# Optimization experiments

Hardware: AMD Instinct MI355X
Metric: run time of the kernel (lower is better)

## Reference

```python
import jax, jax.numpy as jnp
import numpy as np

D_MODEL = 1024
NUM_HEADS = 16
DEPTH = D_MODEL // NUM_HEADS
B, S = 2, 2048


def setup_inputs() -> dict:
    key = jax.random.key(0)
    ks = jax.random.split(key, 11)
    sc = 1.0 / np.sqrt(D_MODEL)
    inp = {
        "q": jax.random.normal(ks[0], (B, S, D_MODEL), jnp.float32),
        "k": jax.random.normal(ks[1], (B, S, D_MODEL), jnp.float32),
        "v": jax.random.normal(ks[2], (B, S, D_MODEL), jnp.float32),
        # 1 = masked (upper triangle), broadcastable to [B,H,S,S]
        "mask": jnp.triu(jnp.ones((S, S), jnp.float32), k=1)[None, None],
        "wq": jax.random.normal(ks[3], (D_MODEL, D_MODEL), jnp.float32) * sc,
        "bq": jnp.zeros((D_MODEL,), jnp.float32),
        "wk": jax.random.normal(ks[4], (D_MODEL, D_MODEL), jnp.float32) * sc,
        "bk": jnp.zeros((D_MODEL,), jnp.float32),
        "wv": jax.random.normal(ks[5], (D_MODEL, D_MODEL), jnp.float32) * sc,
        "bv": jnp.zeros((D_MODEL,), jnp.float32),
        "wo": jax.random.normal(ks[6], (D_MODEL, D_MODEL), jnp.float32) * sc,
        "bo": jnp.zeros((D_MODEL,), jnp.float32),
    }
    return inp


def _split_heads(x):
    b, s, _ = x.shape
    return x.reshape(b, s, NUM_HEADS, DEPTH).transpose(0, 2, 1, 3)  # [B,H,S,D]


def reference(q, k, v, mask, wq, bq, wk, bk, wv, bv, wo, bo):
    qh = _split_heads(q @ wq + bq)
    kh = _split_heads(k @ wk + bk)
    vh = _split_heads(v @ wv + bv)
    logits = jnp.einsum("bhqd,bhkd->bhqk", qh, kh) / jnp.sqrt(
        jnp.asarray(DEPTH, qh.dtype))
    logits = logits + mask * (-1e9)
    attn = jax.nn.softmax(logits, axis=-1)  # [B,H,S,S]
    ctx = jnp.einsum("bhqk,bhkd->bhqd", attn, vh)
    concat = ctx.transpose(0, 2, 1, 3).reshape(q.shape[0], -1, D_MODEL)
    out = concat @ wo + bo
    return out, attn
```

## Files before the change

### kernel.cpp

```cpp
#include <hip/hip_runtime.h>
#include <cstdint>
#include <cstddef>

#define BATCH   2
#define SEQ     2048
#define DMODEL  1024
#define NHEADS  16
#define DHEAD   64
#define TOKENS  (BATCH*SEQ)

typedef __bf16 bf16_t;
typedef bf16_t bf16x8 __attribute__((ext_vector_type(8)));
typedef float  f32x4  __attribute__((ext_vector_type(4)));

__device__ __forceinline__ f32x4 mfma16(bf16x8 a, bf16x8 b, f32x4 c) {
    return __builtin_amdgcn_mfma_f32_16x16x32_bf16(a, b, c, 0, 0, 0);
}

template<int IN_BF16, int MODE>
__global__ __launch_bounds__(256, 2) void proj_gemm(
    const void* __restrict__ xin, const float* __restrict__ W,
    const float* __restrict__ bias, void* __restrict__ out)
{
    __shared__ __align__(16) bf16_t Xl[128*72];
    __shared__ __align__(16) bf16_t Wl[64*72];

    const int t    = threadIdx.x;
    const int w    = t >> 6;
    const int lane = t & 63;
    const int quad = lane >> 4;
    const int l16  = lane & 15;
    const int m0   = blockIdx.y * 128;
    const int n0   = blockIdx.x * 64;

    f32x4 acc[2][4] = {};

    for (int kt = 0; kt < DMODEL/64; ++kt) {
        __syncthreads();
        #pragma unroll
        for (int it = 0; it < 4; ++it) {
            int s   = t + it*256;
            int row = s >> 3, seg = s & 7;
            if (IN_BF16) {
                const bf16_t* xb = (const bf16_t*)xin + (size_t)(m0+row)*DMODEL + kt*64 + seg*8;
                *(bf16x8*)&Xl[row*72 + seg*8] = *(const bf16x8*)xb;
            } else {
                const float* xf = (const float*)xin + (size_t)(m0+row)*DMODEL + kt*64 + seg*8;
                float4 u0 = *(const float4*)xf;
                float4 u1 = *(const float4*)(xf + 4);
                bf16x8 vv;
                vv[0]=(bf16_t)u0.x; vv[1]=(bf16_t)u0.y; vv[2]=(bf16_t)u0.z; vv[3]=(bf16_t)u0.w;
                vv[4]=(bf16_t)u1.x; vv[5]=(bf16_t)u1.y; vv[6]=(bf16_t)u1.z; vv[7]=(bf16_t)u1.w;
                *(bf16x8*)&Xl[row*72 + seg*8] = vv;
            }
        }
        #pragma unroll
        for (int it = 0; it < 2; ++it) {
            int s    = t + it*256;
            int k    = s & 63;
            int nseg = s >> 6;
            const float* wp = W + (size_t)(kt*64 + k)*DMODEL + n0 + nseg*8;
            float4 u0 = *(const float4*)wp;
            float4 u1 = *(const float4*)(wp + 4);
            float f[8] = {u0.x,u0.y,u0.z,u0.w,u1.x,u1.y,u1.z,u1.w};
            #pragma unroll
            for (int j = 0; j < 8; ++j)
                Wl[(nseg*8 + j)*72 + k] = (bf16_t)f[j];
        }
        __syncthreads();

        #pragma unroll
        for (int kk = 0; kk < 2; ++kk) {
            bf16x8 a0 = *(const bf16x8*)&Xl[(w*32      + l16)*72 + kk*32 + quad*8];
            bf16x8 a1 = *(const bf16x8*)&Xl[(w*32 + 16 + l16)*72 + kk*32 + quad*8];
            #pragma unroll
            for (int c = 0; c < 4; ++c) {
                bf16x8 b = *(const bf16x8*)&Wl[(c*16 + l16)*72 + kk*32 + quad*8];
                acc[0][c] = mfma16(a0, b, acc[0][c]);
                acc[1][c] = mfma16(a1, b, acc[1][c]);
            }
        }
    }

    #pragma unroll
    for (int r = 0; r < 2; ++r) {
        #pragma unroll
        for (int c = 0; c < 4; ++c) {
            int n = n0 + c*16 + l16;
            float bv = bias[n];
            #pragma unroll
            for (int reg = 0; reg < 4; ++reg) {
                int gm = m0 + w*32 + r*16 + quad*4 + reg;
                float val = acc[r][c][reg] + bv;
                if (MODE == 2) {
                    ((float*)out)[(size_t)gm*DMODEL + n] = val;
                } else {
                    int b = gm >> 11, sTok = gm & (SEQ-1);
                    int h = n >> 6,  d    = n & (DHEAD-1);
                    if (MODE == 0)
                        ((bf16_t*)out)[(((size_t)(b*NHEADS + h))*SEQ + sTok)*DHEAD + d] = (bf16_t)val;
                    else
                        ((bf16_t*)out)[(((size_t)(b*NHEADS + h))*DHEAD + d)*SEQ + sTok] = (bf16_t)val;
                }
            }
        }
    }
}

__global__ __launch_bounds__(256, 2) void attn_kernel(
    const bf16_t* __restrict__ Qh, const bf16_t* __restrict__ Kh,
    const bf16_t* __restrict__ Vt, float* __restrict__ attn,
    bf16_t* __restrict__ ctx)
{
    __shared__ __align__(16) bf16_t Ql[64*72];
    __shared__ __align__(16) bf16_t Kl[64*72];
    __shared__ __align__(16) bf16_t Vl[64*72];
    __shared__ __align__(16) bf16_t Pl[4][16*72];

    const int t    = threadIdx.x;
    const int w    = t >> 6;
    const int lane = t & 63;
    const int quad = lane >> 4;
    const int l16  = lane & 15;
    const int bh   = blockIdx.y;
    const int q0   = blockIdx.x * 64;

    const bf16_t* Qp = Qh + (size_t)bh * SEQ * DHEAD;
    const bf16_t* Kp = Kh + (size_t)bh * SEQ * DHEAD;
    const bf16_t* Vp = Vt + (size_t)bh * DHEAD * SEQ;
    float* attp = attn + (size_t)bh * SEQ * SEQ;

    #pragma unroll
    for (int it = 0; it < 2; ++it) {
        int s = t + it*256;
        int row = s >> 3, seg = s & 7;
        *(bf16x8*)&Ql[row*72 + seg*8] =
            *(const bf16x8*)(Qp + (size_t)(q0 + row)*DHEAD + seg*8);
    }
    __syncthreads();
    bf16x8 aq[2];
    aq[0] = *(const bf16x8*)&Ql[(w*16 + l16)*72 +      quad*8];
    aq[1] = *(const bf16x8*)&Ql[(w*16 + l16)*72 + 32 + quad*8];

    const int nkt = q0/64 + 1;
    const int qrow_base = q0 + w*16 + quad*4;

    float mrow[4] = {-1e30f, -1e30f, -1e30f, -1e30f};
    float lrow[4] = {0.f, 0.f, 0.f, 0.f};

    for (int kt = 0; kt < nkt; ++kt) {
        __syncthreads();
        #pragma unroll
        for (int it = 0; it < 2; ++it) {
            int s = t + it*256;
            int row = s >> 3, seg = s & 7;
            *(bf16x8*)&Kl[row*72 + seg*8] =
                *(const bf16x8*)(Kp + (size_t)(kt*64 + row)*DHEAD + seg*8);
        }
        __syncthreads();

        f32x4 sf[4] = {};
        #pragma unroll
        for (int kk = 0; kk < 2; ++kk) {
            #pragma unroll
            for (int c = 0; c < 4; ++c) {
                bf16x8 b = *(const bf16x8*)&Kl[(c*16 + l16)*72 + kk*32 + quad*8];
                sf[c] = mfma16(aq[kk], b, sf[c]);
            }
        }
        #pragma unroll
        for (int c = 0; c < 4; ++c) {
            int col = kt*64 + c*16 + l16;
            #pragma unroll
            for (int reg = 0; reg < 4; ++reg) {
                float sv = sf[c][reg] * 0.125f;
                if (col > qrow_base + reg) sv = -1e30f;
                sf[c][reg] = sv;
            }
        }
        #pragma unroll
        for (int reg = 0; reg < 4; ++reg) {
            float tm = fmaxf(fmaxf(sf[0][reg], sf[1][reg]), fmaxf(sf[2][reg], sf[3][reg]));
            #pragma unroll
            for (int msk = 1; msk < 16; msk <<= 1) tm = fmaxf(tm, __shfl_xor(tm, msk));
            float mnew = fmaxf(mrow[reg], tm);
            float ps = __expf(sf[0][reg] - mnew) + __expf(sf[1][reg] - mnew)
                     + __expf(sf[2][reg] - mnew) + __expf(sf[3][reg] - mnew);
            #pragma unroll
            for (int msk = 1; msk < 16; msk <<= 1) ps += __shfl_xor(ps, msk);
            lrow[reg] = lrow[reg] * __expf(mrow[reg] - mnew) + ps;
            mrow[reg] = mnew;
        }
    }

    float invl[4];
    #pragma unroll
    for (int reg = 0; reg < 4; ++reg) invl[reg] = 1.0f / lrow[reg];

    f32x4 cacc[4] = {};
    bf16_t* Plw = &Pl[w][0];

    for (int kt = 0; kt < nkt; ++kt) {
        __syncthreads();
        #pragma unroll
        for (int it = 0; it < 2; ++it) {
            int s = t + it*256;
            int row = s >> 3, seg = s & 7;
            *(bf16x8*)&Kl[row*72 + seg*8] =
                *(const bf16x8*)(Kp + (size_t)(kt*64 + row)*DHEAD + seg*8);
            *(bf16x8*)&Vl[row*72 + seg*8] =
                *(const bf16x8*)(Vp + (size_t)row*SEQ + kt*64 + seg*8);
        }
        __syncthreads();

        f32x4 sf[4] = {};
        #pragma unroll
        for (int kk = 0; kk < 2; ++kk) {
            #pragma unroll
            for (int c = 0; c < 4; ++c) {
                bf16x8 b = *(const bf16x8*)&Kl[(c*16 + l16)*72 + kk*32 + quad*8];
                sf[c] = mfma16(aq[kk], b, sf[c]);
            }
        }
        #pragma unroll
        for (int c = 0; c < 4; ++c) {
            int col = kt*64 + c*16 + l16;
            #pragma unroll
            for (int reg = 0; reg < 4; ++reg) {
                float sv = sf[c][reg] * 0.125f;
                float p  = (col > qrow_base + reg)
                             ? 0.0f
                             : __expf(sv - mrow[reg]) * invl[reg];
                attp[(size_t)(qrow_base + reg)*SEQ + col] = p;
                Plw[(quad*4 + reg)*72 + c*16 + l16] = (bf16_t)p;
            }
        }
        #pragma unroll
        for (int kk = 0; kk < 2; ++kk) {
            bf16x8 ap = *(const bf16x8*)&Plw[l16*72 + kk*32 + quad*8];
            #pragma unroll
            for (int c = 0; c < 4; ++c) {
                bf16x8 bv = *(const bf16x8*)&Vl[(c*16 + l16)*72 + kk*32 + quad*8];
                cacc[c] = mfma16(ap, bv, cacc[c]);
            }
        }
    }

    {
        int r = t >> 2;
        int c4base = nkt*16 + (t & 3);
        float4 z = make_float4(0.f, 0.f, 0.f, 0.f);
        float* rowp = attp + (size_t)(q0 + r)*SEQ;
        for (int c4 = c4base; c4 < SEQ/4; c4 += 4)
            ((float4*)rowp)[c4] = z;
    }

    const int b = bh >> 4, h = bh & 15;
    #pragma unroll
    for (int c = 0; c < 4; ++c) {
        #pragma unroll
        for (int reg = 0; reg < 4; ++reg) {
            int gq = qrow_base + reg;
            size_t idx = ((size_t)(b*SEQ + gq))*DMODEL + h*DHEAD + c*16 + l16;
            ctx[idx] = (bf16_t)cacc[c][reg];
        }
    }
}

extern "C" void kernel_launch(void* const* d_in, const int* in_sizes, int n_in,
                              void* d_out, int out_size, void* d_ws, size_t ws_size,
                              hipStream_t stream) {
    const float* q  = (const float*)d_in[0];
    const float* k  = (const float*)d_in[1];
    const float* v  = (const float*)d_in[2];
    const float* wq = (const float*)d_in[4];
    const float* bq = (const float*)d_in[5];
    const float* wk = (const float*)d_in[6];
    const float* bk = (const float*)d_in[7];
    const float* wv = (const float*)d_in[8];
    const float* bv = (const float*)d_in[9];
    const float* wo = (const float*)d_in[10];
    const float* bo = (const float*)d_in[11];

    float* out  = (float*)d_out;
    float* attn = out + (size_t)TOKENS * DMODEL;

    bf16_t* Qws = (bf16_t*)d_ws;
    bf16_t* Kws = Qws + (size_t)TOKENS * DMODEL;
    bf16_t* Vws = Kws + (size_t)TOKENS * DMODEL;
    bf16_t* Cws = Vws + (size_t)TOKENS * DMODEL;

    dim3 blk(256);
    dim3 gproj(DMODEL/64, TOKENS/128);
    proj_gemm<0,0><<<gproj, blk, 0, stream>>>(q, wq, bq, Qws);
    proj_gemm<0,0><<<gproj, blk, 0, stream>>>(k, wk, bk, Kws);
    proj_gemm<0,1><<<gproj, blk, 0, stream>>>(v, wv, bv, Vws);

    dim3 gattn(SEQ/64, BATCH*NHEADS);
    attn_kernel<<<gattn, blk, 0, stream>>>(Qws, Kws, Vws, attn, Cws);

    proj_gemm<1,2><<<gproj, blk, 0, stream>>>(Cws, wo, bo, out);
}
```

Baseline: 938.7 us.

## Pre-transpose weights to bf16, transpose QK tile layout, use exp2 and nontemporal stores

Adds a conv_w kernel that converts each fp32 weight matrix to a transposed bf16 copy, so the projection GEMMs can load W tiles with vectorized bf16x8 loads instead of a scalar-scatter fp32 conversion. The attention kernel swaps the MFMA operands so each lane owns a single query row. This cuts the row max/sum reductions to two shuffles, lets softmax use exp2f with a prescaled constant, and lets attention probabilities be written as float4 nontemporal stores. Scratch space for the converted weights reuses the attn output buffer and the Q workspace, which adds four small extra kernel launches and relies on ordering so that data is not overwritten while still in use.

Result: no change. 937.9 us (-0.1%).

```diff
diff --git a/kernel.cpp b/kernel.cpp
--- a/kernel.cpp
+++ b/kernel.cpp
@@ -11,15 +11,46 @@
 
 typedef __bf16 bf16_t;
 typedef bf16_t bf16x8 __attribute__((ext_vector_type(8)));
+typedef bf16_t bf16x4 __attribute__((ext_vector_type(4)));
 typedef float  f32x4  __attribute__((ext_vector_type(4)));
 
 __device__ __forceinline__ f32x4 mfma16(bf16x8 a, bf16x8 b, f32x4 c) {
     return __builtin_amdgcn_mfma_f32_16x16x32_bf16(a, b, c, 0, 0, 0);
 }
 
+__global__ __launch_bounds__(256) void conv_w(
+    const float* __restrict__ W, bf16_t* __restrict__ Wt)
+{
+    __shared__ bf16_t tl[64][65];
+    const int t  = threadIdx.x;
+    const int kb = blockIdx.y * 64;
+    const int nb = blockIdx.x * 64;
+    const int r  = t >> 2;
+    const int cs = (t & 3) * 16;
+
+    const float* src = W + (size_t)(kb + r)*DMODEL + nb + cs;
+    #pragma unroll
+    for (int j = 0; j < 4; ++j) {
+        float4 u = ((const float4*)src)[j];
+        tl[r][cs + j*4 + 0] = (bf16_t)u.x;
+        tl[r][cs + j*4 + 1] = (bf16_t)u.y;
+        tl[r][cs + j*4 + 2] = (bf16_t)u.z;
+        tl[r][cs + j*4 + 3] = (bf16_t)u.w;
+    }
+    __syncthreads();
+    bf16_t* dst = Wt + (size_t)(nb + r)*DMODEL + kb + cs;
+    #pragma unroll
+    for (int h = 0; h < 2; ++h) {
+        bf16x8 o;
+        #pragma unroll
+        for (int j = 0; j < 8; ++j) o[j] = tl[cs + h*8 + j][r];
+        *(bf16x8*)(dst + h*8) = o;
+    }
+}
+
 template<int IN_BF16, int MODE>
 __global__ __launch_bounds__(256, 2) void proj_gemm(
-    const void* __restrict__ xin, const float* __restrict__ W,
+    const void* __restrict__ xin, const bf16_t* __restrict__ Wt,
     const float* __restrict__ bias, void* __restrict__ out)
 {
     __shared__ __align__(16) bf16_t Xl[128*72];
@@ -56,16 +87,10 @@
         }
         #pragma unroll
         for (int it = 0; it < 2; ++it) {
-            int s    = t + it*256;
-            int k    = s & 63;
-            int nseg = s >> 6;
-            const float* wp = W + (size_t)(kt*64 + k)*DMODEL + n0 + nseg*8;
-            float4 u0 = *(const float4*)wp;
-            float4 u1 = *(const float4*)(wp + 4);
-            float f[8] = {u0.x,u0.y,u0.z,u0.w,u1.x,u1.y,u1.z,u1.w};
-            #pragma unroll
-            for (int j = 0; j < 8; ++j)
-                Wl[(nseg*8 + j)*72 + k] = (bf16_t)f[j];
+            int s = t + it*256;
+            int n = s >> 3, seg = s & 7;
+            *(bf16x8*)&Wl[n*72 + seg*8] =
+                *(const bf16x8*)(Wt + (size_t)(n0+n)*DMODEL + kt*64 + seg*8);
         }
         __syncthreads();
 
@@ -138,15 +163,15 @@
             *(const bf16x8*)(Qp + (size_t)(q0 + row)*DHEAD + seg*8);
     }
     __syncthreads();
-    bf16x8 aq[2];
-    aq[0] = *(const bf16x8*)&Ql[(w*16 + l16)*72 +      quad*8];
-    aq[1] = *(const bf16x8*)&Ql[(w*16 + l16)*72 + 32 + quad*8];
-
-    const int nkt = q0/64 + 1;
-    const int qrow_base = q0 + w*16 + quad*4;
-
-    float mrow[4] = {-1e30f, -1e30f, -1e30f, -1e30f};
-    float lrow[4] = {0.f, 0.f, 0.f, 0.f};
+    bf16x8 bq[2];
+    bq[0] = *(const bf16x8*)&Ql[(w*16 + l16)*72 +      quad*8];
+    bq[1] = *(const bf16x8*)&Ql[(w*16 + l16)*72 + 32 + quad*8];
+
+    const int nkt  = q0/64 + 1;
+    const int qrow = q0 + w*16 + l16;
+    const float C1 = 0.18033688011112042f;
+
+    float m2 = -1e30f, l2 = 0.f;
 
     for (int kt = 0; kt < nkt; ++kt) {
         __syncthreads();
@@ -164,38 +189,37 @@
         for (int kk = 0; kk < 2; ++kk) {
             #pragma unroll
             for (int c = 0; c < 4; ++c) {
-                bf16x8 b = *(const bf16x8*)&Kl[(c*16 + l16)*72 + kk*32 + quad*8];
-                sf[c] = mfma16(aq[kk], b, sf[c]);
-            }
-        }
+                bf16x8 ak = *(const bf16x8*)&Kl[(c*16 + l16)*72 + kk*32 + quad*8];
+                sf[c] = mfma16(ak, bq[kk], sf[c]);
+            }
+        }
+        float tm = -1e30f;
         #pragma unroll
         for (int c = 0; c < 4; ++c) {
-            int col = kt*64 + c*16 + l16;
+            int colb = kt*64 + c*16 + quad*4;
             #pragma unroll
             for (int reg = 0; reg < 4; ++reg) {
-                float sv = sf[c][reg] * 0.125f;
-                if (col > qrow_base + reg) sv = -1e30f;
-                sf[c][reg] = sv;
-            }
-        }
-        #pragma unroll
-        for (int reg = 0; reg < 4; ++reg) {
-            float tm = fmaxf(fmaxf(sf[0][reg], sf[1][reg]), fmaxf(sf[2][reg], sf[3][reg]));
-            #pragma unroll
-            for (int msk = 1; msk < 16; msk <<= 1) tm = fmaxf(tm, __shfl_xor(tm, msk));
-            float mnew = fmaxf(mrow[reg], tm);
-            float ps = __expf(sf[0][reg] - mnew) + __expf(sf[1][reg] - mnew)
-                     + __expf(sf[2][reg] - mnew) + __expf(sf[3][reg] - mnew);
-            #pragma unroll
-            for (int msk = 1; msk < 16; msk <<= 1) ps += __shfl_xor(ps, msk);
-            lrow[reg] = lrow[reg] * __expf(mrow[reg] - mnew) + ps;
-            mrow[reg] = mnew;
-        }
-    }
-
-    float invl[4];
-    #pragma unroll
-    for (int reg = 0; reg < 4; ++reg) invl[reg] = 1.0f / lrow[reg];
+                float z = sf[c][reg] * C1;
+                z = (colb + reg > qrow) ? -1e30f : z;
+                sf[c][reg] = z;
+                tm = fmaxf(tm, z);
+            }
+        }
+        tm = fmaxf(tm, __shfl_xor(tm, 16));
+        tm = fmaxf(tm, __shfl_xor(tm, 32));
+        float mnew = fmaxf(m2, tm);
+        float ps = 0.f;
+        #pragma unroll
+        for (int c = 0; c < 4; ++c)
+            #pragma unroll
+            for (int reg = 0; reg < 4; ++reg)
+                ps += exp2f(sf[c][reg] - mnew);
+        ps += __shfl_xor(ps, 16);
+        ps += __shfl_xor(ps, 32);
+        l2 = l2 * exp2f(m2 - mnew) + ps;
+        m2 = mnew;
+    }
+    const float invl = 1.0f / l2;
 
     f32x4 cacc[4] = {};
     bf16_t* Plw = &Pl[w][0];
@@ -218,22 +242,26 @@
         for (int kk = 0; kk < 2; ++kk) {
             #pragma unroll
             for (int c = 0; c < 4; ++c) {
-                bf16x8 b = *(const bf16x8*)&Kl[(c*16 + l16)*72 + kk*32 + quad*8];
-                sf[c] = mfma16(aq[kk], b, sf[c]);
+                bf16x8 ak = *(const bf16x8*)&Kl[(c*16 + l16)*72 + kk*32 + quad*8];
+                sf[c] = mfma16(ak, bq[kk], sf[c]);
             }
         }
         #pragma unroll
         for (int c = 0; c < 4; ++c) {
-            int col = kt*64 + c*16 + l16;
+            int colb = kt*64 + c*16 + quad*4;
+            f32x4 pv;
             #pragma unroll
             for (int reg = 0; reg < 4; ++reg) {
-                float sv = sf[c][reg] * 0.125f;
-                float p  = (col > qrow_base + reg)
-                             ? 0.0f
-                             : __expf(sv - mrow[reg]) * invl[reg];
-                attp[(size_t)(qrow_base + reg)*SEQ + col] = p;
-                Plw[(quad*4 + reg)*72 + c*16 + l16] = (bf16_t)p;
-            }
+                float z = sf[c][reg] * C1;
+                float p = (colb + reg > qrow) ? 0.0f : exp2f(z - m2) * invl;
+                pv[reg] = p;
+            }
+            __builtin_nontemporal_store(pv,
+                (f32x4*)(attp + (size_t)qrow*SEQ + colb));
+            bf16x4 pk;
+            pk[0]=(bf16_t)pv[0]; pk[1]=(bf16_t)pv[1];
+            pk[2]=(bf16_t)pv[2]; pk[3]=(bf16_t)pv[3];
+            *(bf16x4*)&Plw[l16*72 + c*16 + quad*4] = pk;
         }
         #pragma unroll
         for (int kk = 0; kk < 2; ++kk) {
@@ -247,12 +275,12 @@
     }
 
     {
-        int r = t >> 2;
-        int c4base = nkt*16 + (t & 3);
-        float4 z = make_float4(0.f, 0.f, 0.f, 0.f);
+        const int r = t >> 2;
+        const int c4base = nkt*16 + (t & 3);
+        f32x4 z = {0.f, 0.f, 0.f, 0.f};
         float* rowp = attp + (size_t)(q0 + r)*SEQ;
         for (int c4 = c4base; c4 < SEQ/4; c4 += 4)
-            ((float4*)rowp)[c4] = z;
+            __builtin_nontemporal_store(z, (f32x4*)rowp + c4);
     }
 
     const int b = bh >> 4, h = bh & 15;
@@ -260,7 +288,7 @@
     for (int c = 0; c < 4; ++c) {
         #pragma unroll
         for (int reg = 0; reg < 4; ++reg) {
-            int gq = qrow_base + reg;
+            int gq = q0 + w*16 + quad*4 + reg;
             size_t idx = ((size_t)(b*SEQ + gq))*DMODEL + h*DHEAD + c*16 + l16;
             ctx[idx] = (bf16_t)cacc[c][reg];
         }
@@ -290,14 +318,23 @@
     bf16_t* Vws = Kws + (size_t)TOKENS * DMODEL;
     bf16_t* Cws = Vws + (size_t)TOKENS * DMODEL;
 
+    bf16_t* WtA = (bf16_t*)attn;
+    bf16_t* WtB = Qws;
+
     dim3 blk(256);
+    dim3 gconv(DMODEL/64, DMODEL/64);
     dim3 gproj(DMODEL/64, TOKENS/128);
-    proj_gemm<0,0><<<gproj, blk, 0, stream>>>(q, wq, bq, Qws);
-    proj_gemm<0,0><<<gproj, blk, 0, stream>>>(k, wk, bk, Kws);
-    proj_gemm<0,1><<<gproj, blk, 0, stream>>>(v, wv, bv, Vws);
+
+    conv_w<<<gconv, blk, 0, stream>>>(wq, WtA);
+    proj_gemm<0,0><<<gproj, blk, 0, stream>>>(q, WtA, bq, Qws);
+    conv_w<<<gconv, blk, 0, stream>>>(wk, WtA);
+    proj_gemm<0,0><<<gproj, blk, 0, stream>>>(k, WtA, bk, Kws);
+    conv_w<<<gconv, blk, 0, stream>>>(wv, WtA);
+    proj_gemm<0,1><<<gproj, blk, 0, stream>>>(v, WtA, bv, Vws);
 
     dim3 gattn(SEQ/64, BATCH*NHEADS);
     attn_kernel<<<gattn, blk, 0, stream>>>(Qws, Kws, Vws, attn, Cws);
 
-    proj_gemm<1,2><<<gproj, blk, 0, stream>>>(Cws, wo, bo, out);
-}
+    conv_w<<<gconv, blk, 0, stream>>>(wo, WtB);
+    proj_gemm<1,2><<<gproj, blk, 0, stream>>>(Cws, WtB, bo, out);
+}
```
